# Optimization experiments

Hardware: AMD Instinct MI355X
Metric: run time of the kernel (lower is better)

## Reference

```python
import jax, jax.numpy as jnp
import numpy as np

NODES_PER_GRAPH = 21
N_GRAPHS = 50_000
N = N_GRAPHS * NODES_PER_GRAPH      # 1,050,000 nodes
E = 2_100_000                        # directed edges
NUM_CLASSES = 26


def setup_inputs() -> dict:
    key = jax.random.key(0)
    ks = jax.random.split(key, 8)
    x = jax.random.normal(ks[0], (N, 2), dtype=jnp.float32)
    src = jax.random.randint(ks[1], (E,), 0, N, dtype=jnp.int32)
    dst = jax.random.randint(ks[2], (E,), 0, N, dtype=jnp.int32)
    batch = (jnp.arange(N, dtype=jnp.int32) // NODES_PER_GRAPH)
    W1 = jax.random.normal(ks[3], (2, 64), dtype=jnp.float32) * 0.5
    b1 = jnp.zeros((64,), dtype=jnp.float32)
    W2 = jax.random.normal(ks[4], (64, 128), dtype=jnp.float32) * 0.125
    b2 = jnp.zeros((128,), dtype=jnp.float32)
    Wfc = jax.random.normal(ks[5], (128, 26), dtype=jnp.float32) * 0.088
    bfc = jnp.zeros((26,), dtype=jnp.float32)
    return {"x": x, "src": src, "dst": dst, "batch": batch,
            "W1": W1, "b1": b1, "W2": W2, "b2": b2, "Wfc": Wfc, "bfc": bfc}


def _gcn_conv(x, W, b, src_l, dst_l, norm, n_nodes):
    # PyG GCNConv: linear transform, then normalized scatter-add aggregation, then bias.
    xw = x @ W                                # [N, F_out]
    msg = xw[src_l] * norm[:, None]           # gather + scale per edge (incl. self-loops)
    out = jax.ops.segment_sum(msg, dst_l, num_segments=n_nodes)
    return out + b


def reference(x, src, dst, batch, W1, b1, W2, b2, Wfc, bfc):
    n = x.shape[0]
    loops = jnp.arange(n, dtype=src.dtype)
    # add self-loops (GCNConv default add_self_loops=True)
    src_l = jnp.concatenate([src, loops])
    dst_l = jnp.concatenate([dst, loops])
    # symmetric normalization: deg over target nodes, norm_e = d^-1/2[src] * d^-1/2[dst]
    deg = jax.ops.segment_sum(jnp.ones_like(dst_l, dtype=x.dtype), dst_l, num_segments=n)
    dinv = jnp.where(deg > 0, jax.lax.rsqrt(deg), 0.0)
    norm = dinv[src_l] * dinv[dst_l]

    h = jax.nn.relu(_gcn_conv(x, W1, b1, src_l, dst_l, norm, n))
    # F.dropout with training=False in eval mode -> identity
    h = _gcn_conv(h, W2, b2, src_l, dst_l, norm, n)

    # global_mean_pool over batch assignment
    n_graphs = N_GRAPHS
    sums = jax.ops.segment_sum(h, batch, num_segments=n_graphs)
    cnts = jax.ops.segment_sum(jnp.ones((n,), dtype=h.dtype), batch, num_segments=n_graphs)
    pooled = sums / jnp.maximum(cnts, 1.0)[:, None]   # [G, 128]

    logits = pooled @ Wfc + bfc
    return jax.nn.log_softmax(logits, axis=1)
```

## Files before the change

### kernel.cpp

```cpp
#include <hip/hip_runtime.h>
#include <hip/hip_fp16.h>
#include <math.h>

#define NODES   1050000
#define EDGES   2100000
#define GRAPHS  50000
#define NPG     21
#define NCLS    26
#define REC_MAX 168

#define NBUCK   1024
#define GPB     49
#define NPB     (GPB*NPG)
#define BCAP    2816
#define NBLK_A  256
#define NTHR_A  1024
#define NTHR_H  1024
#define EPB     ((EDGES + NBLK_A - 1) / NBLK_A)

#define WAVE_FENCE() do { \
    asm volatile("s_waitcnt lgkmcnt(0)" ::: "memory"); \
    __builtin_amdgcn_sched_barrier(0); \
} while (0)

static __device__ __forceinline__ __half2 h2relu(__half2 h) {
    unsigned int u = *reinterpret_cast<unsigned int*>(&h);
    unsigned int r;
    asm("v_pk_max_f16 %0, %1, %2" : "=v"(r) : "v"(u), "v"(0u));
    return *reinterpret_cast<__half2*>(&r);
}

typedef _Float16 hf2 __attribute__((ext_vector_type(2)));
static __device__ __forceinline__ float fdot2(__half2 a, __half2 b, float c) {
#if __has_builtin(__builtin_amdgcn_fdot2)
    return __builtin_amdgcn_fdot2(*reinterpret_cast<hf2*>(&a),
                                  *reinterpret_cast<hf2*>(&b), c, false);
#else
    float2 fa = __half22float2(a), fb = __half22float2(b);
    return fmaf(fa.x, fb.x, fmaf(fa.y, fb.y, c));
#endif
}
static __device__ __forceinline__ float fdot2u(unsigned int a, unsigned int b, float c) {
    return fdot2(*reinterpret_cast<__half2*>(&a), *reinterpret_cast<__half2*>(&b), c);
}

__global__ void __launch_bounds__(NTHR_A) bucket_k(const int* __restrict__ src,
                                                   const int* __restrict__ dst,
                                                   int* __restrict__ bcnt,
                                                   unsigned int* __restrict__ arena) {
    __shared__ int hist[NBUCK];
    __shared__ int gbase[NBUCK];
    int tid = threadIdx.x;
    for (int b = tid; b < NBUCK; b += NTHR_A) hist[b] = 0;
    __syncthreads();
    int e0 = blockIdx.x * EPB;
    int e1 = e0 + EPB; if (e1 > EDGES) e1 = EDGES;
    for (int e = e0 + tid; e < e1; e += NTHR_A) {
        int g = dst[e] / NPG;
        atomicAdd(&hist[g / GPB], 1);
    }
    __syncthreads();
    for (int b = tid; b < NBUCK; b += NTHR_A) {
        int h = hist[b];
        gbase[b] = h ? atomicAdd(&bcnt[b], h) : 0;
        hist[b] = 0;
    }
    __syncthreads();
    for (int e = e0 + tid; e < e1; e += NTHR_A) {
        int s = src[e], d = dst[e];
        int g = d / NPG;
        int b = g / GPB;
        int r = atomicAdd(&hist[b], 1);
        int pos = gbase[b] + r;
        if (pos < BCAP)
            arena[(size_t)b * BCAP + pos] =
                ((unsigned int)s << 11) | ((unsigned int)(g - b * GPB) << 5)
                | (unsigned int)(d - g * NPG);
    }
}

__global__ void __launch_bounds__(NTHR_H) histplace_k(const int* __restrict__ bcnt,
                                                      const unsigned int* __restrict__ arena,
                                                      const float* __restrict__ x,
                                                      int* __restrict__ ecnt,
                                                      int* __restrict__ eoff,
                                                      int* __restrict__ pe,
                                                      float* __restrict__ dinv,
                                                      unsigned int* __restrict__ up,
                                                      const float* __restrict__ W2,
                                                      const float* __restrict__ b2,
                                                      const float* __restrict__ Wfc,
                                                      const float* __restrict__ bfc,
                                                      float* __restrict__ wcomb,
                                                      float* __restrict__ bcomb,
                                                      unsigned int* __restrict__ wch) {
    int b = blockIdx.x, tid = threadIdx.x;
    if (b == NBUCK) {
        for (int t = tid; t < 64 * NCLS + NCLS; t += NTHR_H) {
            if (t < 64 * NCLS) {
                int f = t / NCLS, c = t % NCLS;
                float acc = 0.f;
                for (int k = 0; k < 128; ++k) acc += W2[f * 128 + k] * Wfc[k * NCLS + c];
                wcomb[t] = acc;
            } else {
                int c = t - 64 * NCLS;
                float acc = bfc[c];
                for (int k = 0; k < 128; ++k) acc += b2[k] * Wfc[k * NCLS + c];
                bcomb[c] = acc;
            }
        }
        __syncthreads();
        for (int t = tid; t < 32 * NCLS; t += NTHR_H) {
            int fp = t / NCLS, c = t % NCLS;
            __half2 hh = __floats2half2_rn(wcomb[(2 * fp) * NCLS + c],
                                           wcomb[(2 * fp + 1) * NCLS + c]);
            wch[t] = *reinterpret_cast<unsigned int*>(&hh);
        }
        return;
    }
    __shared__ int h[NPB];
    __shared__ int gsum[GPB];
    __shared__ int go[GPB];
    int lane = tid & 63, wv = tid >> 6;
    for (int i = tid; i < NPB; i += NTHR_H) h[i] = 0;
    __syncthreads();
    int n = bcnt[b]; if (n > BCAP) n = BCAP;
    const unsigned int* ar = arena + (size_t)b * BCAP;
    for (int i = tid; i < n; i += NTHR_H) {
        unsigned int rec = ar[i];
        atomicAdd(&h[((rec >> 5) & 63) * NPG + (rec & 31)], 1);
    }
    __syncthreads();
    int nb0 = b * NPB;
    for (int i = tid; i < NPB; i += NTHR_H) {
        int node = nb0 + i;
        if (node < NODES) {
            float d = 1.0f / sqrtf((float)(h[i] + 1));
            dinv[node] = d;
            float2 xv = ((const float2*)x)[node];
            __half2 hh = __floats2half2_rn(d * xv.x, d * xv.y);
            up[node] = *reinterpret_cast<unsigned int*>(&hh);
        }
    }
    if (tid < GPB) {
        int s = 0;
        #pragma unroll
        for (int k = 0; k < NPG; ++k) s += h[tid * NPG + k];
        gsum[tid] = s;
    }
    __syncthreads();
    if (wv == 0) {
        int cnt = (lane < GPB) ? gsum[lane] : 0;
        int v = cnt;
        #pragma unroll
        for (int o = 1; o < 64; o <<= 1) { int t = __shfl_up(v, o, 64); if (lane >= o) v += t; }
        if (lane < GPB) {
            int st = b * BCAP + (v - cnt);
            go[lane] = st;
            int g = b * GPB + lane;
            if (g < GRAPHS) { ecnt[g] = cnt; eoff[g] = st; }
        }
    }
    __syncthreads();
    for (int i = tid; i < n; i += NTHR_H) {
        unsigned int rec = ar[i];
        int pos = atomicAdd(&go[(rec >> 5) & 63], 1);
        pe[pos] = (int)(((rec >> 11) << 5) | (rec & 31));
    }
}

__global__ void conv1_k(const int* __restrict__ pe, const int* __restrict__ eoff,
                        const int* __restrict__ ecnt, const unsigned int* __restrict__ up,
                        const float* __restrict__ dinv, unsigned int* __restrict__ zh) {
    __shared__ float a1loc[4][NPG][2];
    int lane = threadIdx.x & 63, wv = threadIdx.x >> 6;
    int g    = blockIdx.x * 4 + wv;
    int base = g * NPG;
    if (lane < 2 * NPG) {
        int n = lane >> 1, c = lane & 1;
        unsigned int raw = up[base + n];
        __half2 h = *reinterpret_cast<__half2*>(&raw);
        float2 uv = __half22float2(h);
        a1loc[wv][n][c] = c ? uv.y : uv.x;
    }
    WAVE_FENCE();
    int off = eoff[g], cg = ecnt[g];
    for (int i = lane; i < cg; i += 64) {
        int p = __builtin_nontemporal_load(&pe[off + i]);
        unsigned int raw = up[p >> 5];
        __half2 h = *reinterpret_cast<__half2*>(&raw);
        float2 uv = __half22float2(h);
        atomicAdd(&a1loc[wv][p & 31][0], uv.x);
        atomicAdd(&a1loc[wv][p & 31][1], uv.y);
    }
    WAVE_FENCE();
    if (lane < NPG) {
        float dv = dinv[base + lane];
        int kk = (int)(1.0f / (dv * dv) + 0.5f);
        if (kk > 63) kk = 63;
        __half2 h = __floats2half2_rn(dv * a1loc[wv][lane][0],
                                      dv * a1loc[wv][lane][1]);
        unsigned int zb = *reinterpret_cast<unsigned int*>(&h);
        unsigned int lo = ((zb & 0xFFFFu) + 4u) & 0xFFF8u;
        unsigned int hi = (((zb >> 16) & 0xFFFFu) + 4u) & 0xFFF8u;
        zh[base + lane] = (lo | (unsigned int)(kk & 7))
                        | ((hi | (unsigned int)(kk >> 3)) << 16);
    }
}

__global__ void conv2pool_k(const int* __restrict__ pe, const int* __restrict__ eoff,
                            const int* __restrict__ ecnt,
                            const unsigned int* __restrict__ zh,
                            const float* __restrict__ dinv,
                            const float* __restrict__ W1, const float* __restrict__ b1,
                            const unsigned int* __restrict__ wch,
                            const float* __restrict__ bcomb,
                            float* __restrict__ out) {
    __shared__ unsigned short zxl[4][REC_MAX];
    __shared__ unsigned short zyl[4][REC_MAX];
    __shared__ unsigned short cfl[4][REC_MAX];
    __shared__ float ps[4][64];
    __shared__ unsigned int ps2[4][32];
    __shared__ unsigned int lwch[32 * NCLS];
    int tid = threadIdx.x;
    int lane = tid & 63, wv = tid >> 6;
    for (int i = tid; i < 32 * NCLS; i += 256) lwch[i] = wch[i];
    __syncthreads();

    int g    = blockIdx.x * 4 + wv;
    int base = g * NPG;
    int off  = eoff[g];
    int cg   = ecnt[g];
    if (cg > REC_MAX - NPG) cg = REC_MAX - NPG;

    for (int i = lane; i < cg; i += 64) {
        int p = __builtin_nontemporal_load(&pe[off + i]);
        unsigned int raw = zh[p >> 5];
        unsigned int kk = (raw & 7u) | (((raw >> 16) & 7u) << 3);
        float ds = rsqrtf((float)kk);
        float dd = dinv[base + (p & 31)];
        zxl[wv][i] = (unsigned short)(raw & 0xFFF8u);
        zyl[wv][i] = (unsigned short)((raw >> 16) & 0xFFF8u);
        __half cf = __float2half(ds * dd);
        cfl[wv][i] = *reinterpret_cast<unsigned short*>(&cf);
    }
    int nrec  = cg + NPG;
    int nrec8 = (nrec + 7) & ~7;
    if (lane < NPG) {
        unsigned int raw = zh[base + lane];
        unsigned int kk = (raw & 7u) | (((raw >> 16) & 7u) << 3);
        int i = cg + lane;
        zxl[wv][i] = (unsigned short)(raw & 0xFFF8u);
        zyl[wv][i] = (unsigned short)((raw >> 16) & 0xFFF8u);
        __half cf = __float2half(1.0f / (float)kk);
        cfl[wv][i] = *reinterpret_cast<unsigned short*>(&cf);
    } else if (lane - NPG < nrec8 - nrec) {
        int i = nrec + (lane - NPG);
        zxl[wv][i] = 0;
        zyl[wv][i] = 0;
        cfl[wv][i] = 0;
    }
    WAVE_FENCE();

    const __half2 w0h = __float2half2_rn(W1[lane]);
    const __half2 w1h = __float2half2_rn(W1[64 + lane]);
    const __half2 bbh = __float2half2_rn(b1[lane]);
    float acc = 0.f;
    const uint4* px = (const uint4*)zxl[wv];
    const uint4* py = (const uint4*)zyl[wv];
    const uint4* pc = (const uint4*)cfl[wv];
    int n8 = nrec8 >> 3;
    for (int r = 0; r < n8; ++r) {
        uint4 X = px[r], Y = py[r], C = pc[r];
        {
            __half2 zx = *reinterpret_cast<__half2*>(&X.x);
            __half2 zy = *reinterpret_cast<__half2*>(&Y.x);
            __half2 cf = *reinterpret_cast<__half2*>(&C.x);
            acc = fdot2(h2relu(__hfma2(zx, w0h, __hfma2(zy, w1h, bbh))), cf, acc);
        }
        {
            __half2 zx = *reinterpret_cast<__half2*>(&X.y);
            __half2 zy = *reinterpret_cast<__half2*>(&Y.y);
            __half2 cf = *reinterpret_cast<__half2*>(&C.y);
            acc = fdot2(h2relu(__hfma2(zx, w0h, __hfma2(zy, w1h, bbh))), cf, acc);
        }
        {
            __half2 zx = *reinterpret_cast<__half2*>(&X.z);
            __half2 zy = *reinterpret_cast<__half2*>(&Y.z);
            __half2 cf = *reinterpret_cast<__half2*>(&C.z);
            acc = fdot2(h2relu(__hfma2(zx, w0h, __hfma2(zy, w1h, bbh))), cf, acc);
        }
        {
            __half2 zx = *reinterpret_cast<__half2*>(&X.w);
            __half2 zy = *reinterpret_cast<__half2*>(&Y.w);
            __half2 cf = *reinterpret_cast<__half2*>(&C.w);
            acc = fdot2(h2relu(__hfma2(zx, w0h, __hfma2(zy, w1h, bbh))), cf, acc);
        }
    }
    ps[wv][lane] = acc * (1.0f / (float)NPG);
    WAVE_FENCE();

    if (lane < 32) {
        float2 rp = *reinterpret_cast<float2*>(&ps[wv][2 * lane]);
        __half2 hh = __floats2half2_rn(rp.x, rp.y);
        ps2[wv][lane] = *reinterpret_cast<unsigned int*>(&hh);
    }
    WAVE_FENCE();

    float part = 0.f;
    if (lane < 52) {
        int c  = (lane < NCLS) ? lane : lane - NCLS;
        int f0 = (lane < NCLS) ? 0 : 16;
        #pragma unroll
        for (int fp = 0; fp < 16; ++fp)
            part = fdot2u(ps2[wv][f0 + fp], lwch[(f0 + fp) * NCLS + c], part);
    }
    float other = __shfl(part, lane + NCLS, 64);
    float logit = 0.f;
    if (lane < NCLS) logit = bcomb[lane] + part + other;

    float m = (lane < NCLS) ? logit : -INFINITY;
    #pragma unroll
    for (int o = 32; o; o >>= 1) m = fmaxf(m, __shfl_xor(m, o, 64));
    float ex = (lane < NCLS) ? expf(logit - m) : 0.f;
    float s = ex;
    #pragma unroll
    for (int o = 32; o; o >>= 1) s += __shfl_xor(s, o, 64);
    if (lane < NCLS) out[g * NCLS + lane] = logit - m - logf(s);
}

extern "C" void kernel_launch(void* const* d_in, const int* in_sizes, int n_in,
                              void* d_out, int out_size, void* d_ws, size_t ws_size,
                              hipStream_t stream) {
    const float* x   = (const float*)d_in[0];
    const int*   src = (const int*)  d_in[1];
    const int*   dst = (const int*)  d_in[2];
    const float* W1  = (const float*)d_in[4];
    const float* b1  = (const float*)d_in[5];
    const float* W2  = (const float*)d_in[6];
    const float* b2  = (const float*)d_in[7];
    const float* Wfc = (const float*)d_in[8];
    const float* bfc = (const float*)d_in[9];
    float* out = (float*)d_out;

    char* ws = (char*)d_ws;
    size_t off = 0;
    auto carve = [&](size_t bytes) { char* p = ws + off; off += (bytes + 255) & ~(size_t)255; return p; };
    int*           ecnt  = (int*)           carve((size_t)GRAPHS * 4);
    int*           eoff  = (int*)           carve((size_t)GRAPHS * 4);
    int*           bcnt  = (int*)           carve((size_t)NBUCK * 4);
    float*         dinv  = (float*)         carve((size_t)NODES * 4);
    unsigned int*  up    = (unsigned int*)  carve((size_t)NODES * 4);
    unsigned int*  zh    = (unsigned int*)  carve((size_t)NODES * 4);
    int*           pe    = (int*)           carve((size_t)NBUCK * BCAP * 4);
    unsigned int*  arena = (unsigned int*)  carve((size_t)NBUCK * BCAP * 4);
    float*         wcomb = (float*)         carve((size_t)64 * NCLS * 4);
    float*         bcomb = (float*)         carve((size_t)NCLS * 4);
    unsigned int*  wch   = (unsigned int*)  carve((size_t)32 * NCLS * 4);
    (void)ws_size;

    hipMemsetAsync(bcnt, 0, (size_t)NBUCK * 4, stream);

    bucket_k   <<<NBLK_A, NTHR_A, 0, stream>>>(src, dst, bcnt, arena);
    histplace_k<<<NBUCK + 1, NTHR_H, 0, stream>>>(bcnt, arena, x, ecnt, eoff, pe,
                                                  dinv, up, W2, b2, Wfc, bfc,
                                                  wcomb, bcomb, wch);
    conv1_k    <<<GRAPHS / 4, 256, 0, stream>>>(pe, eoff, ecnt, up, dinv, zh);
    conv2pool_k<<<GRAPHS / 4, 256, 0, stream>>>(pe, eoff, ecnt, zh, dinv, W1, b1,
                                                wch, bcomb, out);
}
```

Measured before the change: 139.0 us.

## Sort edges per destination node and make conv1 a node-parallel CSR gather

The placement kernel now runs a per-node exclusive scan inside each bucket, so edges are grouped by destination node rather than only by graph. It writes a packed per-node offset and degree array. conv1 becomes one thread per node that sums its in-neighbours' features in registers, replacing per-graph waves with LDS float atomics. The cost is extra scan work and syncs in histplace, plus one more node-sized array; degree is clamped to 255 in the packing, and conv2pool still reads per-graph offsets that now point into node-sorted order.

```diff
diff --git a/kernel.cpp b/kernel.cpp
--- a/kernel.cpp
+++ b/kernel.cpp
@@ -12,6 +12,7 @@
 #define NBUCK   1024
 #define GPB     49
 #define NPB     (GPB*NPG)
+#define NPB_PAD 1088
 #define BCAP    2816
 #define NBLK_A  256
 #define NTHR_A  1024
@@ -85,6 +86,7 @@
                                                       int* __restrict__ ecnt,
                                                       int* __restrict__ eoff,
                                                       int* __restrict__ pe,
+                                                      int* __restrict__ nfo,
                                                       float* __restrict__ dinv,
                                                       unsigned int* __restrict__ up,
                                                       const float* __restrict__ W2,
@@ -119,8 +121,9 @@
         return;
     }
     __shared__ int h[NPB];
+    __shared__ int go2[NPB_PAD];
+    __shared__ int wtot[17];
     __shared__ int gsum[GPB];
-    __shared__ int go[GPB];
     int lane = tid & 63, wv = tid >> 6;
     for (int i = tid; i < NPB; i += NTHR_H) h[i] = 0;
     __syncthreads();
@@ -148,64 +151,84 @@
         for (int k = 0; k < NPG; ++k) s += h[tid * NPG + k];
         gsum[tid] = s;
     }
-    __syncthreads();
-    if (wv == 0) {
-        int cnt = (lane < GPB) ? gsum[lane] : 0;
-        int v = cnt;
+    for (int c = wv; c < 17; c += 16) {
+        int idx = c * 64 + lane;
+        int val = (idx < NPB) ? h[idx] : 0;
+        int v = val;
         #pragma unroll
         for (int o = 1; o < 64; o <<= 1) { int t = __shfl_up(v, o, 64); if (lane >= o) v += t; }
-        if (lane < GPB) {
-            int st = b * BCAP + (v - cnt);
-            go[lane] = st;
-            int g = b * GPB + lane;
-            if (g < GRAPHS) { ecnt[g] = cnt; eoff[g] = st; }
-        }
+        go2[idx] = v - val;
+        if (lane == 63) wtot[c] = v;
+    }
+    __syncthreads();
+    if (wv == 0) {
+        int val = (lane < 17) ? wtot[lane] : 0;
+        int v = val;
+        #pragma unroll
+        for (int o = 1; o < 32; o <<= 1) { int t = __shfl_up(v, o, 64); if (lane >= o) v += t; }
+        if (lane < 17) wtot[lane] = v - val;
+    }
+    __syncthreads();
+    for (int i = tid; i < NPB; i += NTHR_H) {
+        int f = go2[i] + wtot[i >> 6];
+        go2[i] = f;
+        int node = nb0 + i;
+        int deg = h[i] > 255 ? 255 : h[i];
+        if (node < NODES) nfo[node] = (f << 8) | deg;
+    }
+    __syncthreads();
+    if (wv == 0 && lane < GPB) {
+        int g = b * GPB + lane;
+        if (g < GRAPHS) { eoff[g] = b * BCAP + go2[lane * NPG]; ecnt[g] = gsum[lane]; }
     }
     __syncthreads();
     for (int i = tid; i < n; i += NTHR_H) {
         unsigned int rec = ar[i];
-        int pos = atomicAdd(&go[(rec >> 5) & 63], 1);
+        int idx = ((rec >> 5) & 63) * NPG + (rec & 31);
+        int pos = b * BCAP + atomicAdd(&go2[idx], 1);
         pe[pos] = (int)(((rec >> 11) << 5) | (rec & 31));
     }
 }
 
-__global__ void conv1_k(const int* __restrict__ pe, const int* __restrict__ eoff,
-                        const int* __restrict__ ecnt, const unsigned int* __restrict__ up,
-                        const float* __restrict__ dinv, unsigned int* __restrict__ zh) {
-    __shared__ float a1loc[4][NPG][2];
-    int lane = threadIdx.x & 63, wv = threadIdx.x >> 6;
-    int g    = blockIdx.x * 4 + wv;
-    int base = g * NPG;
-    if (lane < 2 * NPG) {
-        int n = lane >> 1, c = lane & 1;
-        unsigned int raw = up[base + n];
-        __half2 h = *reinterpret_cast<__half2*>(&raw);
-        float2 uv = __half22float2(h);
-        a1loc[wv][n][c] = c ? uv.y : uv.x;
-    }
-    WAVE_FENCE();
-    int off = eoff[g], cg = ecnt[g];
-    for (int i = lane; i < cg; i += 64) {
-        int p = __builtin_nontemporal_load(&pe[off + i]);
-        unsigned int raw = up[p >> 5];
-        __half2 h = *reinterpret_cast<__half2*>(&raw);
-        float2 uv = __half22float2(h);
-        atomicAdd(&a1loc[wv][p & 31][0], uv.x);
-        atomicAdd(&a1loc[wv][p & 31][1], uv.y);
-    }
-    WAVE_FENCE();
-    if (lane < NPG) {
-        float dv = dinv[base + lane];
-        int kk = (int)(1.0f / (dv * dv) + 0.5f);
-        if (kk > 63) kk = 63;
-        __half2 h = __floats2half2_rn(dv * a1loc[wv][lane][0],
-                                      dv * a1loc[wv][lane][1]);
-        unsigned int zb = *reinterpret_cast<unsigned int*>(&h);
-        unsigned int lo = ((zb & 0xFFFFu) + 4u) & 0xFFF8u;
-        unsigned int hi = (((zb >> 16) & 0xFFFFu) + 4u) & 0xFFF8u;
-        zh[base + lane] = (lo | (unsigned int)(kk & 7))
-                        | ((hi | (unsigned int)(kk >> 3)) << 16);
-    }
+__global__ void __launch_bounds__(256) conv1_k(const int* __restrict__ nfo,
+                                               const int* __restrict__ pe,
+                                               const unsigned int* __restrict__ up,
+                                               unsigned int* __restrict__ zh) {
+    int i = blockIdx.x * 256 + threadIdx.x;
+    if (i >= NODES) return;
+    int b = i / NPB;
+    int info = nfo[i];
+    int off = b * BCAP + (info >> 8);
+    int deg = info & 255;
+    unsigned int raw = up[i];
+    __half2 hs = *reinterpret_cast<__half2*>(&raw);
+    float2 a = __half22float2(hs);
+    int j = 0;
+    for (; j + 2 <= deg; j += 2) {
+        int p0 = pe[off + j], p1 = pe[off + j + 1];
+        unsigned int r0 = up[p0 >> 5], r1 = up[p1 >> 5];
+        __half2 h0 = *reinterpret_cast<__half2*>(&r0);
+        __half2 h1 = *reinterpret_cast<__half2*>(&r1);
+        float2 u0 = __half22float2(h0), u1 = __half22float2(h1);
+        a.x += u0.x + u1.x;
+        a.y += u0.y + u1.y;
+    }
+    if (j < deg) {
+        int p0 = pe[off + j];
+        unsigned int r0 = up[p0 >> 5];
+        __half2 h0 = *reinterpret_cast<__half2*>(&r0);
+        float2 u0 = __half22float2(h0);
+        a.x += u0.x;
+        a.y += u0.y;
+    }
+    int kk = deg + 1;
+    float dv = rsqrtf((float)kk);
+    if (kk > 63) kk = 63;
+    __half2 h = __floats2half2_rn(dv * a.x, dv * a.y);
+    unsigned int zb = *reinterpret_cast<unsigned int*>(&h);
+    unsigned int lo = ((zb & 0xFFFFu) + 4u) & 0xFFF8u;
+    unsigned int hi = (((zb >> 16) & 0xFFFFu) + 4u) & 0xFFF8u;
+    zh[i] = (lo | (unsigned int)(kk & 7)) | ((hi | (unsigned int)(kk >> 3)) << 16);
 }
 
 __global__ void conv2pool_k(const int* __restrict__ pe, const int* __restrict__ eoff,
@@ -352,6 +375,7 @@
     float*         dinv  = (float*)         carve((size_t)NODES * 4);
     unsigned int*  up    = (unsigned int*)  carve((size_t)NODES * 4);
     unsigned int*  zh    = (unsigned int*)  carve((size_t)NODES * 4);
+    int*           nfo   = (int*)           carve((size_t)NODES * 4);
     int*           pe    = (int*)           carve((size_t)NBUCK * BCAP * 4);
     unsigned int*  arena = (unsigned int*)  carve((size_t)NBUCK * BCAP * 4);
     float*         wcomb = (float*)         carve((size_t)64 * NCLS * 4);
@@ -362,10 +386,10 @@
     hipMemsetAsync(bcnt, 0, (size_t)NBUCK * 4, stream);
 
     bucket_k   <<<NBLK_A, NTHR_A, 0, stream>>>(src, dst, bcnt, arena);
-    histplace_k<<<NBUCK + 1, NTHR_H, 0, stream>>>(bcnt, arena, x, ecnt, eoff, pe,
+    histplace_k<<<NBUCK + 1, NTHR_H, 0, stream>>>(bcnt, arena, x, ecnt, eoff, pe, nfo,
                                                   dinv, up, W2, b2, Wfc, bfc,
                                                   wcomb, bcomb, wch);
-    conv1_k    <<<GRAPHS / 4, 256, 0, stream>>>(pe, eoff, ecnt, up, dinv, zh);
+    conv1_k    <<<(NODES + 255) / 256, 256, 0, stream>>>(nfo, pe, up, zh);
     conv2pool_k<<<GRAPHS / 4, 256, 0, stream>>>(pe, eoff, ecnt, zh, dinv, W1, b1,
                                                 wch, bcomb, out);
 }
```

Result: faster. 127.8 us (-8.1%).
